# Optimization experiments

Measured on AMD Instinct MI355X. Metric: run time of the kernel, lower is better.

Reference implementation:

```python
import jax, jax.numpy as jnp
from jax import lax
import numpy as np

B, T, D, H, C = 256, 2048, 40, 128, 35
LN_EPS = 1e-5


def _uniform(key, shape, scale):
    return jax.random.uniform(key, shape, jnp.float32, -scale, scale)


def setup_inputs() -> dict:
    key = jax.random.key(0)
    ks = jax.random.split(key, 16)
    s = 1.0 / np.sqrt(H)  # PyTorch LSTM init scale
    inp = {
        "x": jax.random.normal(ks[0], (B, T, D), jnp.float32),
        "length": jax.random.randint(ks[1], (B,), 1, T + 1, jnp.int32),
        # layer 0 (input_size=D)
        "W_ih0": _uniform(ks[2], (4 * H, D), s),
        "W_hh0": _uniform(ks[3], (4 * H, H), s),
        "b_ih0": _uniform(ks[4], (4 * H,), s),
        "b_hh0": _uniform(ks[5], (4 * H,), s),
        # layer 1 (input_size=H)
        "W_ih1": _uniform(ks[6], (4 * H, H), s),
        "W_hh1": _uniform(ks[7], (4 * H, H), s),
        "b_ih1": _uniform(ks[8], (4 * H,), s),
        "b_hh1": _uniform(ks[9], (4 * H,), s),
        # LayerNorm + Linear head
        "ln_gamma": jnp.ones((H,), jnp.float32),
        "ln_beta": jnp.zeros((H,), jnp.float32),
        "fc_w": _uniform(ks[10], (C, H), 1.0 / np.sqrt(H)),
        "fc_b": _uniform(ks[11], (C,), 1.0 / np.sqrt(H)),
    }
    return inp


def _lstm_layer(xs, length, W_ih, W_hh, b_ih, b_hh):
    # xs: [T, B, D_in]; masked recurrence emulates pack_padded_sequence:
    # state is frozen for t >= length, so the final h equals the state at
    # each sequence's last valid step.
    Tn, Bn = xs.shape[0], xs.shape[1]
    Hn = W_hh.shape[1]
    h0 = jnp.zeros((Bn, Hn), xs.dtype)
    c0 = jnp.zeros((Bn, Hn), xs.dtype)

    def step(carry, inp):
        h, c = carry
        x_t, t = inp
        gates = x_t @ W_ih.T + b_ih + h @ W_hh.T + b_hh  # [B, 4H]
        i, f, g, o = jnp.split(gates, 4, axis=-1)  # PyTorch gate order i,f,g,o
        i = jax.nn.sigmoid(i)
        f = jax.nn.sigmoid(f)
        g = jnp.tanh(g)
        o = jax.nn.sigmoid(o)
        c_new = f * c + i * g
        h_new = o * jnp.tanh(c_new)
        m = (t < length)[:, None]
        h = jnp.where(m, h_new, h)
        c = jnp.where(m, c_new, c)
        return (h, c), h

    (h_fin, c_fin), hs = lax.scan(step, (h0, c0), (xs, jnp.arange(Tn)))
    return hs, h_fin


def reference(x, length, W_ih0, W_hh0, b_ih0, b_hh0, W_ih1, W_hh1, b_ih1, b_hh1,
              ln_gamma, ln_beta, fc_w, fc_b):
    xs = jnp.transpose(x, (1, 0, 2))  # [T, B, D]
    hs1, _ = _lstm_layer(xs, length, W_ih0, W_hh0, b_ih0, b_hh0)
    _, h_last = _lstm_layer(hs1, length, W_ih1, W_hh1, b_ih1, b_hh1)  # h[-1]: [B, H]
    # LayerNorm over feature dim
    mu = jnp.mean(h_last, axis=-1, keepdims=True)
    var = jnp.mean(jnp.square(h_last - mu), axis=-1, keepdims=True)
    hn = (h_last - mu) * lax.rsqrt(var + LN_EPS) * ln_gamma + ln_beta
    return hn @ fc_w.T + fc_b  # [B, C]
```

## Files before the change

### kernel.cpp

```cpp
#include <hip/hip_runtime.h>

#define Bn 256
#define Tn 2048
#define Dn 40
#define Hn 128
#define Cn 35

typedef _Float16 h2 __attribute__((ext_vector_type(2)));

__device__ __forceinline__ int sdot4(int a, int b, int c) {
#if __has_builtin(__builtin_amdgcn_sdot4)
  return __builtin_amdgcn_sdot4(a, b, c, false);
#else
  int r = c;
#pragma unroll
  for (int i = 0; i < 4; ++i)
    r += ((int)(a << (24 - 8 * i)) >> 24) * ((int)(b << (24 - 8 * i)) >> 24);
  return r;
#endif
}

__device__ __forceinline__ float fdot2f(h2 a, h2 b, float c) {
#if __has_builtin(__builtin_amdgcn_fdot2)
  return __builtin_amdgcn_fdot2(a, b, c, false);
#else
  return c + (float)(a[0]) * (float)(b[0]) + (float)(a[1]) * (float)(b[1]);
#endif
}

__device__ __forceinline__ h2 bch(int u) { return __builtin_bit_cast(h2, u); }

__device__ __forceinline__ int pk2i(float a, float b) {
  h2 r; r[0] = (_Float16)a; r[1] = (_Float16)b;
  return __builtin_bit_cast(int, r);
}

__device__ __forceinline__ float rcpf_(float x) {
#if __has_builtin(__builtin_amdgcn_rcpf)
  return __builtin_amdgcn_rcpf(x);
#else
  return 1.f / x;
#endif
}

__device__ __forceinline__ float sigm(float v) {
  v = fmaxf(fminf(v, 60.f), -60.f);
  return rcpf_(1.f + __expf(-v));
}

__device__ __forceinline__ float tanha(float v) {
  v = fmaxf(fminf(v, 15.f), -15.f);
  const float e = __expf(2.f * v);
  return (e - 1.f) * rcpf_(e + 1.f);
}

__device__ __forceinline__ int q8c(float v) {
  v = fminf(fmaxf(v, -127.f), 127.f);
  return (int)__builtin_rintf(v);
}

__device__ __forceinline__ int pk4(int a, int b, int c, int d) {
  return (a & 255) | ((b & 255) << 8) | ((c & 255) << 16) | (d << 24);
}

#if __has_builtin(__builtin_amdgcn_global_load_lds)
#define HAVE_GLDS 1
__device__ __forceinline__ void gl_lds16(const float* g, float* l) {
  __builtin_amdgcn_global_load_lds(
      (const __attribute__((address_space(1))) unsigned int*)(const void*)g,
      (__attribute__((address_space(3))) unsigned int*)(void*)l, 16, 0, 0);
}
#endif

__device__ __forceinline__ void quantW128(const float* __restrict__ p,
                                          int* __restrict__ q, float& sc) {
  float m = 1e-30f;
#pragma unroll
  for (int i = 0; i < 32; ++i) {
    const float4 v = reinterpret_cast<const float4*>(p)[i];
    m = fmaxf(m, fmaxf(fmaxf(fabsf(v.x), fabsf(v.y)),
                       fmaxf(fabsf(v.z), fabsf(v.w))));
  }
  const float inv = 127.f / m;
  sc = m * (1.f / 127.f);
#pragma unroll
  for (int i = 0; i < 32; ++i) {
    const float4 v = reinterpret_cast<const float4*>(p)[i];
    q[i] = pk4(q8c(v.x * inv), q8c(v.y * inv), q8c(v.z * inv), q8c(v.w * inv));
  }
}

#define RLST(w) __builtin_amdgcn_readlane(                                  \
    ((w) < 64 ? st0 : (w) < 128 ? st1 : (w) < 192 ? st2 : (w) < 256 ? st3  \
                                                        : st4), (w) & 63)

__global__ __launch_bounds__(512) void lstm2_fused(
    const float* __restrict__ x,
    const int*   __restrict__ length,
    const float* __restrict__ Wih0, const float* __restrict__ Whh0,
    const float* __restrict__ bih0, const float* __restrict__ bhh0,
    const float* __restrict__ Wih1, const float* __restrict__ Whh1,
    const float* __restrict__ bih1, const float* __restrict__ bhh1,
    const float* __restrict__ gam,  const float* __restrict__ bet,
    const float* __restrict__ fcw,  const float* __restrict__ fcb,
    float* __restrict__ out)
{
  __shared__ int   s_w0x[20][512];
  __shared__ __align__(16) float s_xraw[192 * 4];
  __shared__ int   s_xh2[2][320];
  __shared__ float s_xp[2][16][512];
  __shared__ float s_p0[4][132];
  __shared__ float s_p1[4][132];
  __shared__ int   s_hq[64];
  __shared__ float s_h1f[128];
  __shared__ float s_hn[128];

  const int tid  = threadIdx.x;
  const int lane = tid & 63;
  const int b    = blockIdx.x;
  const int len  = length[b];

  if (tid >= 256 && tid < 448) {
    const int seg0 = (tid >> 6) - 4;
    int seg = seg0 * 64 + lane;
    if (seg >= 160) seg = 0;
#if HAVE_GLDS
    gl_lds16(x + (size_t)b * Tn * Dn + seg * 4, &s_xraw[seg0 * 256]);
#else
    *(float4*)&s_xraw[seg * 4] =
        *(const float4*)(x + (size_t)b * Tn * Dn + seg * 4);
#endif
  }

  int q0h[32], q1x[32], q1h[32];
  float s0h, s1x, s1h;
  quantW128(Whh0 + (size_t)tid * Hn, q0h, s0h);
  quantW128(Wih1 + (size_t)tid * Hn, q1x, s1x);
  quantW128(Whh1 + (size_t)tid * Hn, q1h, s1h);
  s0h *= (1.f / 127.f);
  s1x *= (1.f / 127.f);
  s1h *= (1.f / 127.f);
  {
    const float* p = Wih0 + (size_t)tid * Dn;
#pragma unroll
    for (int k = 0; k < 20; ++k) s_w0x[k][tid] = pk2i(p[2 * k], p[2 * k + 1]);
  }
  const float bias0 = bih0[tid] + bhh0[tid];
  const float bias1 = bih1[tid] + bhh1[tid];

  float c0 = 0.f;
  float c1 = 0.f;

  if (tid < 64) s_hq[tid] = 0;
  __syncthreads();

  auto burst = [&](int bb) {
    const int* flat = &s_xh2[bb][0];
    const int st0 = flat[lane], st1 = flat[lane + 64], st2 = flat[lane + 128],
              st3 = flat[lane + 192], st4 = flat[lane + 256];
#pragma unroll
    for (int pass = 0; pass < 4; ++pass) {
      float a0 = 0.f, a1 = 0.f, a2 = 0.f, a3 = 0.f;
      const int r0 = pass * 4;
#pragma unroll
      for (int g = 0; g < 5; ++g) {
        const h2 w0 = bch(s_w0x[4 * g + 0][tid]);
        const h2 w1 = bch(s_w0x[4 * g + 1][tid]);
        const h2 w2 = bch(s_w0x[4 * g + 2][tid]);
        const h2 w3 = bch(s_w0x[4 * g + 3][tid]);
        a0 = fdot2f(bch(RLST(20 * (r0 + 0) + 4 * g + 0)), w0, a0);
        a0 = fdot2f(bch(RLST(20 * (r0 + 0) + 4 * g + 1)), w1, a0);
        a0 = fdot2f(bch(RLST(20 * (r0 + 0) + 4 * g + 2)), w2, a0);
        a0 = fdot2f(bch(RLST(20 * (r0 + 0) + 4 * g + 3)), w3, a0);
        a1 = fdot2f(bch(RLST(20 * (r0 + 1) + 4 * g + 0)), w0, a1);
        a1 = fdot2f(bch(RLST(20 * (r0 + 1) + 4 * g + 1)), w1, a1);
        a1 = fdot2f(bch(RLST(20 * (r0 + 1) + 4 * g + 2)), w2, a1);
        a1 = fdot2f(bch(RLST(20 * (r0 + 1) + 4 * g + 3)), w3, a1);
        a2 = fdot2f(bch(RLST(20 * (r0 + 2) + 4 * g + 0)), w0, a2);
        a2 = fdot2f(bch(RLST(20 * (r0 + 2) + 4 * g + 1)), w1, a2);
        a2 = fdot2f(bch(RLST(20 * (r0 + 2) + 4 * g + 2)), w2, a2);
        a2 = fdot2f(bch(RLST(20 * (r0 + 2) + 4 * g + 3)), w3, a2);
        a3 = fdot2f(bch(RLST(20 * (r0 + 3) + 4 * g + 0)), w0, a3);
        a3 = fdot2f(bch(RLST(20 * (r0 + 3) + 4 * g + 1)), w1, a3);
        a3 = fdot2f(bch(RLST(20 * (r0 + 3) + 4 * g + 2)), w2, a3);
        a3 = fdot2f(bch(RLST(20 * (r0 + 3) + 4 * g + 3)), w3, a3);
      }
      s_xp[bb][r0 + 0][tid] = a0;
      s_xp[bb][r0 + 1][tid] = a1;
      s_xp[bb][r0 + 2][tid] = a2;
      s_xp[bb][r0 + 3][tid] = a3;
    }
  };

  if (tid >= 256 && tid < 416) {
    const int u = tid - 256;
    const float4 v = *(const float4*)&s_xraw[4 * u];
    s_xh2[0][2 * u]     = pk2i(v.x, v.y);
    s_xh2[0][2 * u + 1] = pk2i(v.z, v.w);
  }
  __syncthreads();
  burst(0);
  __syncthreads();
  s_p0[tid >> 7][tid & 127] = bias0 + s_xp[0][0][tid];
  __syncthreads();

#pragma unroll 1
  for (int t = 0; t < len; ++t) {
    const int tl = t & 15;

    if (tid < 128) {
      const float gi = s_p0[0][tid], gf = s_p0[1][tid];
      const float gg = s_p0[2][tid], go = s_p0[3][tid];
      c0 = sigm(gf) * c0 + sigm(gi) * tanha(gg);
      const float h = sigm(go) * tanha(c0);
      ((signed char*)s_hq)[tid] = (signed char)(int)__builtin_rintf(h * 127.f);
    } else if (tid < 256) {
      if (t > 0) {
        const int u = tid - 128;
        const float gi = s_p1[0][u], gf = s_p1[1][u];
        const float gg = s_p1[2][u], go = s_p1[3][u];
        c1 = sigm(gf) * c1 + sigm(gi) * tanha(gg);
        const float h = sigm(go) * tanha(c1);
        ((signed char*)s_hq)[128 + u] =
            (signed char)(int)__builtin_rintf(h * 127.f);
      }
    } else if (tid < 416 && tl == 13) {
      const int u = tid - 256;
      const float4 v = *(const float4*)&s_xraw[4 * u];
      const int nb = ((t + 3) >> 4) & 1;
      s_xh2[nb][2 * u]     = pk2i(v.x, v.y);
      s_xh2[nb][2 * u + 1] = pk2i(v.z, v.w);
    }
    __syncthreads();

    const int vq = s_hq[lane];

    if (tid >= 256 && tid < 448 && tl == 12) {
      const int t0 = (t & ~15) + 16;
      if (t0 <= Tn - 16) {
        const int seg0 = (tid >> 6) - 4;
        int seg = seg0 * 64 + lane;
        if (seg >= 160) seg = 0;
#if HAVE_GLDS
        gl_lds16(x + ((size_t)b * Tn + t0) * Dn + seg * 4,
                 &s_xraw[seg0 * 256]);
#else
        *(float4*)&s_xraw[seg * 4] =
            *(const float4*)(x + ((size_t)b * Tn + t0) * Dn + seg * 4);
#endif
      }
    }

    const int rowi = t + 1;
    const float xacc = s_xp[(rowi >> 4) & 1][rowi & 15][tid];

    int ia = 0, ia2 = 0, ib = 0, ib2 = 0, ic = 0, ic2 = 0;
#pragma unroll
    for (int j = 0; j < 32; j += 2) {
      const int s0 = __builtin_amdgcn_readlane(vq, j);
      const int s1 = __builtin_amdgcn_readlane(vq, j + 1);
      ia  = sdot4(s0, q0h[j], ia);
      ib  = sdot4(s0, q1x[j], ib);
      ia2 = sdot4(s1, q0h[j + 1], ia2);
      ib2 = sdot4(s1, q1x[j + 1], ib2);
    }
#pragma unroll
    for (int j = 0; j < 32; j += 2) {
      const int s0 = __builtin_amdgcn_readlane(vq, 32 + j);
      const int s1 = __builtin_amdgcn_readlane(vq, 33 + j);
      ic  = sdot4(s0, q1h[j], ic);
      ic2 = sdot4(s1, q1h[j + 1], ic2);
    }
    s_p0[tid >> 7][tid & 127] = bias0 + xacc + (float)(ia + ia2) * s0h;
    s_p1[tid >> 7][tid & 127] =
        bias1 + (float)(ib + ib2) * s1x + (float)(ic + ic2) * s1h;

    if (tl == 14) burst(((t + 2) >> 4) & 1);
    __syncthreads();
  }

  if (tid >= 128 && tid < 256) {
    const int u = tid - 128;
    const float gi = s_p1[0][u], gf = s_p1[1][u];
    const float gg = s_p1[2][u], go = s_p1[3][u];
    c1 = sigm(gf) * c1 + sigm(gi) * tanha(gg);
    s_h1f[u] = sigm(go) * tanha(c1);
  }
  __syncthreads();

  if (tid < 64) {
    const float a = s_h1f[tid], d = s_h1f[64 + tid];
    float s = a + d, q = a * a + d * d;
#pragma unroll
    for (int m = 32; m >= 1; m >>= 1) {
      s += __shfl_xor(s, m, 64);
      q += __shfl_xor(q, m, 64);
    }
    const float mu = s * (1.f / 128.f);
    float var = q * (1.f / 128.f) - mu * mu;
    var = fmaxf(var, 0.f);
    const float rstd = rsqrtf(var + 1e-5f);
    s_hn[tid]      = (a - mu) * rstd * gam[tid]      + bet[tid];
    s_hn[64 + tid] = (d - mu) * rstd * gam[64 + tid] + bet[64 + tid];
  }
  __syncthreads();

  if (tid < Cn) {
    float acc = fcb[tid];
    const float* wp = fcw + tid * Hn;
#pragma unroll 4
    for (int k = 0; k < Hn; ++k) acc += s_hn[k] * wp[k];
    out[(size_t)b * Cn + tid] = acc;
  }
}

extern "C" void kernel_launch(void* const* d_in, const int* in_sizes, int n_in,
                              void* d_out, int out_size, void* d_ws, size_t ws_size,
                              hipStream_t stream) {
  (void)in_sizes; (void)n_in; (void)d_ws; (void)ws_size; (void)out_size;
  lstm2_fused<<<dim3(Bn), dim3(512), 0, stream>>>(
      (const float*)d_in[0],  (const int*)d_in[1],
      (const float*)d_in[2],  (const float*)d_in[3],
      (const float*)d_in[4],  (const float*)d_in[5],
      (const float*)d_in[6],  (const float*)d_in[7],
      (const float*)d_in[8],  (const float*)d_in[9],
      (const float*)d_in[10], (const float*)d_in[11],
      (const float*)d_in[12], (const float*)d_in[13],
      (float*)d_out);
}
```

Baseline: 2.512 ms.

## Split LSTM into four warp-specialized wavefronts synced by LDS flags

Replaces the 512-thread block-synchronous step loop with four specialized wavefronts. One runs the layer-0 recurrence, one the layer-1 recurrence, one the layer-1 input projection, and one the x projection with prefetch. They hand off through ring buffers in LDS guarded by spin-polled flags instead of __syncthreads. Each lane holds all four gates for two hidden units, so it applies the nonlinearities itself, and int8 h is packed with DPP. This removes per-step block barriers and lets the two layers run as a pipeline, at the cost of one wave doing 8x the dot products per step and heavy register pressure.

```diff
diff --git a/kernel.cpp b/kernel.cpp
--- a/kernel.cpp
+++ b/kernel.cpp
@@ -61,6 +61,13 @@
 
 __device__ __forceinline__ int pk4(int a, int b, int c, int d) {
   return (a & 255) | ((b & 255) << 8) | ((c & 255) << 16) | (d << 24);
+}
+
+__device__ __forceinline__ int dpp_x1(int v) {
+  return __builtin_amdgcn_update_dpp(0, v, 0xB1, 0xF, 0xF, true);
+}
+__device__ __forceinline__ int dpp_x2(int v) {
+  return __builtin_amdgcn_update_dpp(0, v, 0x4E, 0xF, 0xF, true);
 }
 
 #if __has_builtin(__builtin_amdgcn_global_load_lds)
@@ -94,7 +101,22 @@
     ((w) < 64 ? st0 : (w) < 128 ? st1 : (w) < 192 ? st2 : (w) < 256 ? st3  \
                                                         : st4), (w) & 63)
 
-__global__ __launch_bounds__(512) void lstm2_fused(
+#define MEMBAR() asm volatile("" ::: "memory")
+#define POLL_GE(idx, val, cache)                                             \
+  do {                                                                       \
+    if ((cache) < (val)) {                                                   \
+      do { (cache) = *(volatile int*)&s_flag[idx]; } while ((cache) < (val));\
+    }                                                                        \
+    MEMBAR();                                                                \
+  } while (0)
+#define PUBLISH(idx, val)                                                    \
+  do {                                                                       \
+    MEMBAR();                                                                \
+    asm volatile("s_waitcnt lgkmcnt(0)" ::: "memory");                       \
+    *(volatile int*)&s_flag[idx] = (val);                                    \
+  } while (0)
+
+__global__ __launch_bounds__(256, 1) void lstm2_fused(
     const float* __restrict__ x,
     const int*   __restrict__ length,
     const float* __restrict__ Wih0, const float* __restrict__ Whh0,
@@ -105,187 +127,316 @@
     const float* __restrict__ fcw,  const float* __restrict__ fcb,
     float* __restrict__ out)
 {
-  __shared__ int   s_w0x[20][512];
-  __shared__ __align__(16) float s_xraw[192 * 4];
-  __shared__ int   s_xh2[2][320];
-  __shared__ float s_xp[2][16][512];
-  __shared__ float s_p0[4][132];
-  __shared__ float s_p1[4][132];
-  __shared__ int   s_hq[64];
+  __shared__ __align__(16) float s_xraw[160 * 4];
+  __shared__ int   s_xh2[320];
+  __shared__ float s_xp[2][16][8][64];
+  __shared__ float s_term[4][8][64];
+  __shared__ int   s_h0q[4][32];
+  __shared__ int   s_flag[4];
   __shared__ float s_h1f[128];
   __shared__ float s_hn[128];
 
   const int tid  = threadIdx.x;
   const int lane = tid & 63;
+  const int wv   = tid >> 6;
   const int b    = blockIdx.x;
   const int len  = length[b];
 
-  if (tid >= 256 && tid < 448) {
-    const int seg0 = (tid >> 6) - 4;
-    int seg = seg0 * 64 + lane;
-    if (seg >= 160) seg = 0;
+  if (tid < 4) s_flag[tid] = 0;
+  __syncthreads();
+
+
+  if (wv == 0) {
+    int q0[32], q1[32], q2[32], q3[32], q4[32], q5[32], q6[32], q7[32];
+    float sc[8], bs[8];
+    quantW128(Whh0 + (size_t)(lane)       * Hn, q0, sc[0]);
+    quantW128(Whh0 + (size_t)(lane + 64)  * Hn, q1, sc[1]);
+    quantW128(Whh0 + (size_t)(lane + 128) * Hn, q2, sc[2]);
+    quantW128(Whh0 + (size_t)(lane + 192) * Hn, q3, sc[3]);
+    quantW128(Whh0 + (size_t)(lane + 256) * Hn, q4, sc[4]);
+    quantW128(Whh0 + (size_t)(lane + 320) * Hn, q5, sc[5]);
+    quantW128(Whh0 + (size_t)(lane + 384) * Hn, q6, sc[6]);
+    quantW128(Whh0 + (size_t)(lane + 448) * Hn, q7, sc[7]);
+#pragma unroll
+    for (int k = 0; k < 8; ++k) {
+      sc[k] *= (1.f / 127.f);
+      bs[k] = bih0[lane + 64 * k] + bhh0[lane + 64 * k];
+    }
+    const int shl = 8 * (lane & 3);
+    float cA = 0.f, cB = 0.f;
+    int wA = 0, wB = 0;
+    int fX = 0, fT = 0;
+#pragma unroll 1
+    for (int t = 0; t < len; ++t) {
+      const int tl = t & 15;
+      if (tl == 0) POLL_GE(3, (t >> 4) + 1, fX);
+      POLL_GE(1, t - 3, fT);
+      const float* xb = &s_xp[(t >> 4) & 1][tl][0][lane];
+      float xv0 = xb[0], xv1 = xb[64], xv2 = xb[128], xv3 = xb[192],
+            xv4 = xb[256], xv5 = xb[320], xv6 = xb[384], xv7 = xb[448];
+      int a0 = 0, a1 = 0, a2 = 0, a3 = 0, a4 = 0, a5 = 0, a6 = 0, a7 = 0;
+#pragma unroll
+      for (int j = 0; j < 16; ++j) {
+        const int s = __builtin_amdgcn_readlane(wA, 4 * j);
+        a0 = sdot4(s, q0[j], a0); a1 = sdot4(s, q1[j], a1);
+        a2 = sdot4(s, q2[j], a2); a3 = sdot4(s, q3[j], a3);
+        a4 = sdot4(s, q4[j], a4); a5 = sdot4(s, q5[j], a5);
+        a6 = sdot4(s, q6[j], a6); a7 = sdot4(s, q7[j], a7);
+      }
+#pragma unroll
+      for (int j = 0; j < 16; ++j) {
+        const int s = __builtin_amdgcn_readlane(wB, 4 * j);
+        a0 = sdot4(s, q0[16 + j], a0); a1 = sdot4(s, q1[16 + j], a1);
+        a2 = sdot4(s, q2[16 + j], a2); a3 = sdot4(s, q3[16 + j], a3);
+        a4 = sdot4(s, q4[16 + j], a4); a5 = sdot4(s, q5[16 + j], a5);
+        a6 = sdot4(s, q6[16 + j], a6); a7 = sdot4(s, q7[16 + j], a7);
+      }
+      const float gAi = bs[0] + xv0 + (float)a0 * sc[0];
+      const float gBi = bs[1] + xv1 + (float)a1 * sc[1];
+      const float gAf = bs[2] + xv2 + (float)a2 * sc[2];
+      const float gBf = bs[3] + xv3 + (float)a3 * sc[3];
+      const float gAg = bs[4] + xv4 + (float)a4 * sc[4];
+      const float gBg = bs[5] + xv5 + (float)a5 * sc[5];
+      const float gAo = bs[6] + xv6 + (float)a6 * sc[6];
+      const float gBo = bs[7] + xv7 + (float)a7 * sc[7];
+      cA = sigm(gAf) * cA + sigm(gAi) * tanha(gAg);
+      const float hA = sigm(gAo) * tanha(cA);
+      cB = sigm(gBf) * cB + sigm(gBi) * tanha(gBg);
+      const float hB = sigm(gBo) * tanha(cB);
+      int vA = (((int)__builtin_rintf(hA * 127.f)) & 255) << shl;
+      int vB = (((int)__builtin_rintf(hB * 127.f)) & 255) << shl;
+      vA |= dpp_x1(vA); vA |= dpp_x2(vA);
+      vB |= dpp_x1(vB); vB |= dpp_x2(vB);
+      wA = vA; wB = vB;
+      if ((lane & 3) == 0) {
+        s_h0q[t & 3][lane >> 2]        = vA;
+        s_h0q[t & 3][16 + (lane >> 2)] = vB;
+      }
+      fT = *(volatile int*)&s_flag[1];
+      PUBLISH(0, t + 1);
+    }
+  } else if (wv == 1) {
+    int q0[32], q1[32], q2[32], q3[32], q4[32], q5[32], q6[32], q7[32];
+    float sc[8];
+    quantW128(Whh1 + (size_t)(lane)       * Hn, q0, sc[0]);
+    quantW128(Whh1 + (size_t)(lane + 64)  * Hn, q1, sc[1]);
+    quantW128(Whh1 + (size_t)(lane + 128) * Hn, q2, sc[2]);
+    quantW128(Whh1 + (size_t)(lane + 192) * Hn, q3, sc[3]);
+    quantW128(Whh1 + (size_t)(lane + 256) * Hn, q4, sc[4]);
+    quantW128(Whh1 + (size_t)(lane + 320) * Hn, q5, sc[5]);
+    quantW128(Whh1 + (size_t)(lane + 384) * Hn, q6, sc[6]);
+    quantW128(Whh1 + (size_t)(lane + 448) * Hn, q7, sc[7]);
+#pragma unroll
+    for (int k = 0; k < 8; ++k) sc[k] *= (1.f / 127.f);
+    const int shl = 8 * (lane & 3);
+    float cA = 0.f, cB = 0.f;
+    int wA = 0, wB = 0;
+    int fT = 0;
+#pragma unroll 1
+    for (int t = 0; t < len; ++t) {
+      POLL_GE(1, t + 1, fT);
+      const float* tb = &s_term[t & 3][0][lane];
+      float tv0 = tb[0], tv1 = tb[64], tv2 = tb[128], tv3 = tb[192],
+            tv4 = tb[256], tv5 = tb[320], tv6 = tb[384], tv7 = tb[448];
+      int a0 = 0, a1 = 0, a2 = 0, a3 = 0, a4 = 0, a5 = 0, a6 = 0, a7 = 0;
+#pragma unroll
+      for (int j = 0; j < 16; ++j) {
+        const int s = __builtin_amdgcn_readlane(wA, 4 * j);
+        a0 = sdot4(s, q0[j], a0); a1 = sdot4(s, q1[j], a1);
+        a2 = sdot4(s, q2[j], a2); a3 = sdot4(s, q3[j], a3);
+        a4 = sdot4(s, q4[j], a4); a5 = sdot4(s, q5[j], a5);
+        a6 = sdot4(s, q6[j], a6); a7 = sdot4(s, q7[j], a7);
+      }
+#pragma unroll
+      for (int j = 0; j < 16; ++j) {
+        const int s = __builtin_amdgcn_readlane(wB, 4 * j);
+        a0 = sdot4(s, q0[16 + j], a0); a1 = sdot4(s, q1[16 + j], a1);
+        a2 = sdot4(s, q2[16 + j], a2); a3 = sdot4(s, q3[16 + j], a3);
+        a4 = sdot4(s, q4[16 + j], a4); a5 = sdot4(s, q5[16 + j], a5);
+        a6 = sdot4(s, q6[16 + j], a6); a7 = sdot4(s, q7[16 + j], a7);
+      }
+      const float gAi = tv0 + (float)a0 * sc[0];
+      const float gBi = tv1 + (float)a1 * sc[1];
+      const float gAf = tv2 + (float)a2 * sc[2];
+      const float gBf = tv3 + (float)a3 * sc[3];
+      const float gAg = tv4 + (float)a4 * sc[4];
+      const float gBg = tv5 + (float)a5 * sc[5];
+      const float gAo = tv6 + (float)a6 * sc[6];
+      const float gBo = tv7 + (float)a7 * sc[7];
+      cA = sigm(gAf) * cA + sigm(gAi) * tanha(gAg);
+      const float hA = sigm(gAo) * tanha(cA);
+      cB = sigm(gBf) * cB + sigm(gBi) * tanha(gBg);
+      const float hB = sigm(gBo) * tanha(cB);
+      if (t == len - 1) { s_h1f[lane] = hA; s_h1f[lane + 64] = hB; }
+      int vA = (((int)__builtin_rintf(hA * 127.f)) & 255) << shl;
+      int vB = (((int)__builtin_rintf(hB * 127.f)) & 255) << shl;
+      vA |= dpp_x1(vA); vA |= dpp_x2(vA);
+      vB |= dpp_x1(vB); vB |= dpp_x2(vB);
+      wA = vA; wB = vB;
+      fT = *(volatile int*)&s_flag[1];
+      PUBLISH(2, t + 1);
+    }
+  } else if (wv == 2) {
+    int q0[32], q1[32], q2[32], q3[32], q4[32], q5[32], q6[32], q7[32];
+    float sc[8], bs[8];
+    quantW128(Wih1 + (size_t)(lane)       * Hn, q0, sc[0]);
+    quantW128(Wih1 + (size_t)(lane + 64)  * Hn, q1, sc[1]);
+    quantW128(Wih1 + (size_t)(lane + 128) * Hn, q2, sc[2]);
+    quantW128(Wih1 + (size_t)(lane + 192) * Hn, q3, sc[3]);
+    quantW128(Wih1 + (size_t)(lane + 256) * Hn, q4, sc[4]);
+    quantW128(Wih1 + (size_t)(lane + 320) * Hn, q5, sc[5]);
+    quantW128(Wih1 + (size_t)(lane + 384) * Hn, q6, sc[6]);
+    quantW128(Wih1 + (size_t)(lane + 448) * Hn, q7, sc[7]);
+#pragma unroll
+    for (int k = 0; k < 8; ++k) {
+      sc[k] *= (1.f / 127.f);
+      bs[k] = bih1[lane + 64 * k] + bhh1[lane + 64 * k];
+    }
+    int fL0 = 0, fL1 = 0;
+#pragma unroll 1
+    for (int t = 0; t < len; ++t) {
+      POLL_GE(0, t + 1, fL0);
+      POLL_GE(2, t - 3, fL1);
+      const int vq = s_h0q[t & 3][lane & 31];
+      int a0 = 0, a1 = 0, a2 = 0, a3 = 0, a4 = 0, a5 = 0, a6 = 0, a7 = 0;
+#pragma unroll
+      for (int j = 0; j < 32; ++j) {
+        const int s = __builtin_amdgcn_readlane(vq, j);
+        a0 = sdot4(s, q0[j], a0); a1 = sdot4(s, q1[j], a1);
+        a2 = sdot4(s, q2[j], a2); a3 = sdot4(s, q3[j], a3);
+        a4 = sdot4(s, q4[j], a4); a5 = sdot4(s, q5[j], a5);
+        a6 = sdot4(s, q6[j], a6); a7 = sdot4(s, q7[j], a7);
+      }
+      float* tb = &s_term[t & 3][0][lane];
+      tb[0]   = bs[0] + (float)a0 * sc[0];
+      tb[64]  = bs[1] + (float)a1 * sc[1];
+      tb[128] = bs[2] + (float)a2 * sc[2];
+      tb[192] = bs[3] + (float)a3 * sc[3];
+      tb[256] = bs[4] + (float)a4 * sc[4];
+      tb[320] = bs[5] + (float)a5 * sc[5];
+      tb[384] = bs[6] + (float)a6 * sc[6];
+      tb[448] = bs[7] + (float)a7 * sc[7];
+      fL0 = *(volatile int*)&s_flag[0];
+      fL1 = *(volatile int*)&s_flag[2];
+      PUBLISH(1, t + 1);
+    }
+  } else {
+    int wp0[20], wp1[20], wp2[20], wp3[20], wp4[20], wp5[20], wp6[20], wp7[20];
+    {
+      const float* p;
+      p = Wih0 + (size_t)(lane)       * Dn;
+#pragma unroll
+      for (int w = 0; w < 20; ++w) wp0[w] = pk2i(p[2 * w], p[2 * w + 1]);
+      p = Wih0 + (size_t)(lane + 64)  * Dn;
+#pragma unroll
+      for (int w = 0; w < 20; ++w) wp1[w] = pk2i(p[2 * w], p[2 * w + 1]);
+      p = Wih0 + (size_t)(lane + 128) * Dn;
+#pragma unroll
+      for (int w = 0; w < 20; ++w) wp2[w] = pk2i(p[2 * w], p[2 * w + 1]);
+      p = Wih0 + (size_t)(lane + 192) * Dn;
+#pragma unroll
+      for (int w = 0; w < 20; ++w) wp3[w] = pk2i(p[2 * w], p[2 * w + 1]);
+      p = Wih0 + (size_t)(lane + 256) * Dn;
+#pragma unroll
+      for (int w = 0; w < 20; ++w) wp4[w] = pk2i(p[2 * w], p[2 * w + 1]);
+      p = Wih0 + (size_t)(lane + 320) * Dn;
+#pragma unroll
+      for (int w = 0; w < 20; ++w) wp5[w] = pk2i(p[2 * w], p[2 * w + 1]);
+      p = Wih0 + (size_t)(lane + 384) * Dn;
+#pragma unroll
+      for (int w = 0; w < 20; ++w) wp6[w] = pk2i(p[2 * w], p[2 * w + 1]);
+      p = Wih0 + (size_t)(lane + 448) * Dn;
+#pragma unroll
+      for (int w = 0; w < 20; ++w) wp7[w] = pk2i(p[2 * w], p[2 * w + 1]);
+    }
+    const int nch = (len + 15) >> 4;
+    {
+      const float* src = x + (size_t)b * Tn * Dn;
 #if HAVE_GLDS
-    gl_lds16(x + (size_t)b * Tn * Dn + seg * 4, &s_xraw[seg0 * 256]);
+      gl_lds16(src + lane * 4,        &s_xraw[lane * 4]);
+      gl_lds16(src + (lane + 64) * 4, &s_xraw[(lane + 64) * 4]);
+      if (lane < 32)
+        gl_lds16(src + (lane + 128) * 4, &s_xraw[(lane + 128) * 4]);
+      asm volatile("s_waitcnt vmcnt(0)" ::: "memory");
 #else
-    *(float4*)&s_xraw[seg * 4] =
-        *(const float4*)(x + (size_t)b * Tn * Dn + seg * 4);
-#endif
+      *(float4*)&s_xraw[lane * 4] = *(const float4*)(src + lane * 4);
+      *(float4*)&s_xraw[(lane + 64) * 4] = *(const float4*)(src + (lane + 64) * 4);
+      if (lane < 32)
+        *(float4*)&s_xraw[(lane + 128) * 4] = *(const float4*)(src + (lane + 128) * 4);
+#endif
+      {
+        float4 v = *(const float4*)&s_xraw[4 * lane];
+        s_xh2[2 * lane] = pk2i(v.x, v.y); s_xh2[2 * lane + 1] = pk2i(v.z, v.w);
+        v = *(const float4*)&s_xraw[4 * (lane + 64)];
+        s_xh2[2 * (lane + 64)] = pk2i(v.x, v.y);
+        s_xh2[2 * (lane + 64) + 1] = pk2i(v.z, v.w);
+        if (lane < 32) {
+          v = *(const float4*)&s_xraw[4 * (lane + 128)];
+          s_xh2[2 * (lane + 128)] = pk2i(v.x, v.y);
+          s_xh2[2 * (lane + 128) + 1] = pk2i(v.z, v.w);
+        }
+      }
+    }
+    int fL0 = 0;
+#pragma unroll 1
+    for (int k = 0; k < nch; ++k) {
+      const bool more = (k + 1 < nch);
+      if (more) {
+        const float* src = x + ((size_t)b * Tn + (size_t)(k + 1) * 16) * Dn;
+#if HAVE_GLDS
+        gl_lds16(src + lane * 4,        &s_xraw[lane * 4]);
+        gl_lds16(src + (lane + 64) * 4, &s_xraw[(lane + 64) * 4]);
+        if (lane < 32)
+          gl_lds16(src + (lane + 128) * 4, &s_xraw[(lane + 128) * 4]);
+#else
+        *(float4*)&s_xraw[lane * 4] = *(const float4*)(src + lane * 4);
+        *(float4*)&s_xraw[(lane + 64) * 4] = *(const float4*)(src + (lane + 64) * 4);
+        if (lane < 32)
+          *(float4*)&s_xraw[(lane + 128) * 4] = *(const float4*)(src + (lane + 128) * 4);
+#endif
+      }
+      {
+        const int* flat = s_xh2;
+        const int st0 = flat[lane], st1 = flat[lane + 64],
+                  st2 = flat[lane + 128], st3 = flat[lane + 192],
+                  st4 = flat[lane + 256];
+#pragma unroll 1
+        for (int tl = 0; tl < 16; ++tl) {
+          float a0 = 0.f, a1 = 0.f, a2 = 0.f, a3 = 0.f,
+                a4 = 0.f, a5 = 0.f, a6 = 0.f, a7 = 0.f;
+#pragma unroll
+          for (int w = 0; w < 20; ++w) {
+            const h2 s = bch(RLST(20 * tl + w));
+            a0 = fdot2f(s, bch(wp0[w]), a0); a1 = fdot2f(s, bch(wp1[w]), a1);
+            a2 = fdot2f(s, bch(wp2[w]), a2); a3 = fdot2f(s, bch(wp3[w]), a3);
+            a4 = fdot2f(s, bch(wp4[w]), a4); a5 = fdot2f(s, bch(wp5[w]), a5);
+            a6 = fdot2f(s, bch(wp6[w]), a6); a7 = fdot2f(s, bch(wp7[w]), a7);
+          }
+          float* xb = &s_xp[k & 1][tl][0][lane];
+          xb[0] = a0;   xb[64] = a1;  xb[128] = a2; xb[192] = a3;
+          xb[256] = a4; xb[320] = a5; xb[384] = a6; xb[448] = a7;
+        }
+      }
+      PUBLISH(3, k + 1);
+      if (more) {
+        POLL_GE(0, 16 * k, fL0);
+#if HAVE_GLDS
+        asm volatile("s_waitcnt vmcnt(0)" ::: "memory");
+#endif
+        float4 v = *(const float4*)&s_xraw[4 * lane];
+        s_xh2[2 * lane] = pk2i(v.x, v.y); s_xh2[2 * lane + 1] = pk2i(v.z, v.w);
+        v = *(const float4*)&s_xraw[4 * (lane + 64)];
+        s_xh2[2 * (lane + 64)] = pk2i(v.x, v.y);
+        s_xh2[2 * (lane + 64) + 1] = pk2i(v.z, v.w);
+        if (lane < 32) {
+          v = *(const float4*)&s_xraw[4 * (lane + 128)];
+          s_xh2[2 * (lane + 128)] = pk2i(v.x, v.y);
+          s_xh2[2 * (lane + 128) + 1] = pk2i(v.z, v.w);
+        }
+      }
+    }
   }
 
-  int q0h[32], q1x[32], q1h[32];
-  float s0h, s1x, s1h;
-  quantW128(Whh0 + (size_t)tid * Hn, q0h, s0h);
-  quantW128(Wih1 + (size_t)tid * Hn, q1x, s1x);
-  quantW128(Whh1 + (size_t)tid * Hn, q1h, s1h);
-  s0h *= (1.f / 127.f);
-  s1x *= (1.f / 127.f);
-  s1h *= (1.f / 127.f);
-  {
-    const float* p = Wih0 + (size_t)tid * Dn;
-#pragma unroll
-    for (int k = 0; k < 20; ++k) s_w0x[k][tid] = pk2i(p[2 * k], p[2 * k + 1]);
-  }
-  const float bias0 = bih0[tid] + bhh0[tid];
-  const float bias1 = bih1[tid] + bhh1[tid];
-
-  float c0 = 0.f;
-  float c1 = 0.f;
-
-  if (tid < 64) s_hq[tid] = 0;
-  __syncthreads();
-
-  auto burst = [&](int bb) {
-    const int* flat = &s_xh2[bb][0];
-    const int st0 = flat[lane], st1 = flat[lane + 64], st2 = flat[lane + 128],
-              st3 = flat[lane + 192], st4 = flat[lane + 256];
-#pragma unroll
-    for (int pass = 0; pass < 4; ++pass) {
-      float a0 = 0.f, a1 = 0.f, a2 = 0.f, a3 = 0.f;
-      const int r0 = pass * 4;
-#pragma unroll
-      for (int g = 0; g < 5; ++g) {
-        const h2 w0 = bch(s_w0x[4 * g + 0][tid]);
-        const h2 w1 = bch(s_w0x[4 * g + 1][tid]);
-        const h2 w2 = bch(s_w0x[4 * g + 2][tid]);
-        const h2 w3 = bch(s_w0x[4 * g + 3][tid]);
-        a0 = fdot2f(bch(RLST(20 * (r0 + 0) + 4 * g + 0)), w0, a0);
-        a0 = fdot2f(bch(RLST(20 * (r0 + 0) + 4 * g + 1)), w1, a0);
-        a0 = fdot2f(bch(RLST(20 * (r0 + 0) + 4 * g + 2)), w2, a0);
-        a0 = fdot2f(bch(RLST(20 * (r0 + 0) + 4 * g + 3)), w3, a0);
-        a1 = fdot2f(bch(RLST(20 * (r0 + 1) + 4 * g + 0)), w0, a1);
-        a1 = fdot2f(bch(RLST(20 * (r0 + 1) + 4 * g + 1)), w1, a1);
-        a1 = fdot2f(bch(RLST(20 * (r0 + 1) + 4 * g + 2)), w2, a1);
-        a1 = fdot2f(bch(RLST(20 * (r0 + 1) + 4 * g + 3)), w3, a1);
-        a2 = fdot2f(bch(RLST(20 * (r0 + 2) + 4 * g + 0)), w0, a2);
-        a2 = fdot2f(bch(RLST(20 * (r0 + 2) + 4 * g + 1)), w1, a2);
-        a2 = fdot2f(bch(RLST(20 * (r0 + 2) + 4 * g + 2)), w2, a2);
-        a2 = fdot2f(bch(RLST(20 * (r0 + 2) + 4 * g + 3)), w3, a2);
-        a3 = fdot2f(bch(RLST(20 * (r0 + 3) + 4 * g + 0)), w0, a3);
-        a3 = fdot2f(bch(RLST(20 * (r0 + 3) + 4 * g + 1)), w1, a3);
-        a3 = fdot2f(bch(RLST(20 * (r0 + 3) + 4 * g + 2)), w2, a3);
-        a3 = fdot2f(bch(RLST(20 * (r0 + 3) + 4 * g + 3)), w3, a3);
-      }
-      s_xp[bb][r0 + 0][tid] = a0;
-      s_xp[bb][r0 + 1][tid] = a1;
-      s_xp[bb][r0 + 2][tid] = a2;
-      s_xp[bb][r0 + 3][tid] = a3;
-    }
-  };
-
-  if (tid >= 256 && tid < 416) {
-    const int u = tid - 256;
-    const float4 v = *(const float4*)&s_xraw[4 * u];
-    s_xh2[0][2 * u]     = pk2i(v.x, v.y);
-    s_xh2[0][2 * u + 1] = pk2i(v.z, v.w);
-  }
-  __syncthreads();
-  burst(0);
-  __syncthreads();
-  s_p0[tid >> 7][tid & 127] = bias0 + s_xp[0][0][tid];
-  __syncthreads();
-
-#pragma unroll 1
-  for (int t = 0; t < len; ++t) {
-    const int tl = t & 15;
-
-    if (tid < 128) {
-      const float gi = s_p0[0][tid], gf = s_p0[1][tid];
-      const float gg = s_p0[2][tid], go = s_p0[3][tid];
-      c0 = sigm(gf) * c0 + sigm(gi) * tanha(gg);
-      const float h = sigm(go) * tanha(c0);
-      ((signed char*)s_hq)[tid] = (signed char)(int)__builtin_rintf(h * 127.f);
-    } else if (tid < 256) {
-      if (t > 0) {
-        const int u = tid - 128;
-        const float gi = s_p1[0][u], gf = s_p1[1][u];
-        const float gg = s_p1[2][u], go = s_p1[3][u];
-        c1 = sigm(gf) * c1 + sigm(gi) * tanha(gg);
-        const float h = sigm(go) * tanha(c1);
-        ((signed char*)s_hq)[128 + u] =
-            (signed char)(int)__builtin_rintf(h * 127.f);
-      }
-    } else if (tid < 416 && tl == 13) {
-      const int u = tid - 256;
-      const float4 v = *(const float4*)&s_xraw[4 * u];
-      const int nb = ((t + 3) >> 4) & 1;
-      s_xh2[nb][2 * u]     = pk2i(v.x, v.y);
-      s_xh2[nb][2 * u + 1] = pk2i(v.z, v.w);
-    }
-    __syncthreads();
-
-    const int vq = s_hq[lane];
-
-    if (tid >= 256 && tid < 448 && tl == 12) {
-      const int t0 = (t & ~15) + 16;
-      if (t0 <= Tn - 16) {
-        const int seg0 = (tid >> 6) - 4;
-        int seg = seg0 * 64 + lane;
-        if (seg >= 160) seg = 0;
-#if HAVE_GLDS
-        gl_lds16(x + ((size_t)b * Tn + t0) * Dn + seg * 4,
-                 &s_xraw[seg0 * 256]);
-#else
-        *(float4*)&s_xraw[seg * 4] =
-            *(const float4*)(x + ((size_t)b * Tn + t0) * Dn + seg * 4);
-#endif
-      }
-    }
-
-    const int rowi = t + 1;
-    const float xacc = s_xp[(rowi >> 4) & 1][rowi & 15][tid];
-
-    int ia = 0, ia2 = 0, ib = 0, ib2 = 0, ic = 0, ic2 = 0;
-#pragma unroll
-    for (int j = 0; j < 32; j += 2) {
-      const int s0 = __builtin_amdgcn_readlane(vq, j);
-      const int s1 = __builtin_amdgcn_readlane(vq, j + 1);
-      ia  = sdot4(s0, q0h[j], ia);
-      ib  = sdot4(s0, q1x[j], ib);
-      ia2 = sdot4(s1, q0h[j + 1], ia2);
-      ib2 = sdot4(s1, q1x[j + 1], ib2);
-    }
-#pragma unroll
-    for (int j = 0; j < 32; j += 2) {
-      const int s0 = __builtin_amdgcn_readlane(vq, 32 + j);
-      const int s1 = __builtin_amdgcn_readlane(vq, 33 + j);
-      ic  = sdot4(s0, q1h[j], ic);
-      ic2 = sdot4(s1, q1h[j + 1], ic2);
-    }
-    s_p0[tid >> 7][tid & 127] = bias0 + xacc + (float)(ia + ia2) * s0h;
-    s_p1[tid >> 7][tid & 127] =
-        bias1 + (float)(ib + ib2) * s1x + (float)(ic + ic2) * s1h;
-
-    if (tl == 14) burst(((t + 2) >> 4) & 1);
-    __syncthreads();
-  }
-
-  if (tid >= 128 && tid < 256) {
-    const int u = tid - 128;
-    const float gi = s_p1[0][u], gf = s_p1[1][u];
-    const float gg = s_p1[2][u], go = s_p1[3][u];
-    c1 = sigm(gf) * c1 + sigm(gi) * tanha(gg);
-    s_h1f[u] = sigm(go) * tanha(c1);
-  }
   __syncthreads();
 
   if (tid < 64) {
@@ -318,7 +469,7 @@
                               void* d_out, int out_size, void* d_ws, size_t ws_size,
                               hipStream_t stream) {
   (void)in_sizes; (void)n_in; (void)d_ws; (void)ws_size; (void)out_size;
-  lstm2_fused<<<dim3(Bn), dim3(512), 0, stream>>>(
+  lstm2_fused<<<dim3(Bn), dim3(256), 0, stream>>>(
       (const float*)d_in[0],  (const int*)d_in[1],
       (const float*)d_in[2],  (const float*)d_in[3],
       (const float*)d_in[4],  (const float*)d_in[5],
```

Measured after the change: 2.494 ms. No clear change (-0.7%).
